# Optimization experiments

Hardware: AMD Instinct MI355X
Metric: run time of the kernel (lower is better)

## Reference

```python
import jax, jax.numpy as jnp
import numpy as np

D_INNER = 4096
DT_RANK = 128
D_STATE = 16
SEQ_LEN = 4096


def setup_inputs() -> dict:
    key = jax.random.key(0)
    kx, kin, kdel = jax.random.split(key, 3)
    x = jax.random.normal(kx, (SEQ_LEN, D_INNER), dtype=jnp.float32)
    # eqx.nn.Linear weights are [out_features, in_features]
    lim_in = 1.0 / np.sqrt(D_INNER)
    W_in = jax.random.uniform(kin, (DT_RANK + 2 * D_STATE, D_INNER),
                              minval=-lim_in, maxval=lim_in, dtype=jnp.float32)
    lim_d = 1.0 / np.sqrt(DT_RANK)
    W_delta = jax.random.uniform(kdel, (D_INNER, DT_RANK),
                                 minval=-lim_d, maxval=lim_d, dtype=jnp.float32)
    # A_log init exactly as in the module (deterministic)
    A = jnp.repeat(jnp.arange(1, D_STATE + 1), D_INNER).reshape(D_INNER, D_STATE)
    A_log = jnp.log(A.astype(jnp.float32))
    D = jnp.ones((D_INNER,), dtype=jnp.float32)
    return {"x": x, "W_in": W_in, "W_delta": W_delta, "A_log": A_log, "D": D}


def selective_scan(x, delta, A, B, C, D):
    # x, delta: [L, d_inner]; A: [d_inner, d_state]; B, C: [L, d_state]; D: [d_inner]
    d_inner, d_state = A.shape
    delta_A = jnp.exp(jnp.einsum('ld,dn->ldn', delta, A))          # [L, d_inner, d_state]
    delta_B_u = jnp.einsum('ld,ln,ld->ldn', delta, B, x)           # [L, d_inner, d_state]

    def step(h, inp):
        dA, dBu, c = inp
        h = dA * h + dBu                                           # [d_inner, d_state]
        y = jnp.einsum('dn,n->d', h, c)
        return h, y

    h0 = jnp.zeros((d_inner, d_state), dtype=x.dtype)
    _, ys = jax.lax.scan(step, h0, (delta_A, delta_B_u, C))
    return ys + x * D


def reference(x, W_in, W_delta, A_log, D):
    A = -jnp.exp(A_log)
    dbc = x @ W_in.T                                               # [L, dt_rank + 2*d_state]
    delta, B, C = jnp.split(dbc, [DT_RANK, DT_RANK + D_STATE], axis=-1)
    delta = jax.nn.softplus(delta @ W_delta.T)                     # [L, d_inner]
    return selective_scan(x, delta, A, B, C, D)
```

## Files before the change

### kernel.cpp

```cpp
#include <hip/hip_runtime.h>
#include <math.h>
#include <stdint.h>

#define L_SEQ   4096
#define DI      4096
#define RNK     128
#define NS      16
#define NCOL    160
#define KSPLIT  16

#define DBC_SLICE 655360
#define PART_OFF  655360
#define DSZ       524288
#define WSZ       655360
#define PART_STRIDE (32 * 4096)

typedef __attribute__((ext_vector_type(8))) short bf16x8;
typedef __attribute__((ext_vector_type(4))) float f32x4;

__device__ __forceinline__ float fast_exp2(float v) {
#if __has_builtin(__builtin_amdgcn_exp2f)
  return __builtin_amdgcn_exp2f(v);
#else
  return exp2f(v);
#endif
}

__device__ __forceinline__ unsigned short f2bf(float f) {
  uint32_t u = __float_as_uint(f);
  uint32_t r = (u + 0x7FFFu + ((u >> 16) & 1u)) >> 16;
  return (unsigned short)r;
}
__device__ __forceinline__ float bf2f(unsigned short b) {
  return __uint_as_float(((uint32_t)b) << 16);
}

__global__ __launch_bounds__(256) void split_pair_kernel(const float* __restrict__ src,
                                                         unsigned short* __restrict__ dh,
                                                         unsigned short* __restrict__ dl) {
  const int i = (blockIdx.x * 256 + threadIdx.x) * 4;
  float4 a = *(const float4*)&src[i];
  float v[4] = {a.x, a.y, a.z, a.w};
  ushort4 h, lo;
  unsigned short* hp = (unsigned short*)&h;
  unsigned short* lp = (unsigned short*)&lo;
#pragma unroll
  for (int q = 0; q < 4; ++q) {
    hp[q] = f2bf(v[q]);
    lp[q] = f2bf(v[q] - bf2f(hp[q]));
  }
  *(ushort4*)&dh[i] = h;
  *(ushort4*)&dl[i] = lo;
}

__global__ __launch_bounds__(256) void gemm1_kernel(const float* __restrict__ x,
                                                    const unsigned short* __restrict__ winh,
                                                    const unsigned short* __restrict__ winl,
                                                    float* __restrict__ parts) {
  const int t  = threadIdx.x;
  const int w  = t >> 6, l = t & 63;
  const int lr = l & 15;
  const int lk = l >> 4;
  const int mt = blockIdx.x >> 4;
  const int ks = blockIdx.x & 15;
  const int wr = w >> 1, wc = w & 1;
  const int row = mt * 32 + wr * 16 + lr;
  const int c0  = wc * 80;
  const int kb  = ks * 256;

  f32x4 acc[5];
#pragma unroll
  for (int j = 0; j < 5; ++j) acc[j] = (f32x4){0.f, 0.f, 0.f, 0.f};

#pragma unroll
  for (int kc = 0; kc < 8; ++kc) {
    const int k0 = kb + kc * 32 + lk * 8;
    float4 xa0 = *(const float4*)&x[row * 4096 + k0];
    float4 xa1 = *(const float4*)&x[row * 4096 + k0 + 4];
    float va[8] = {xa0.x, xa0.y, xa0.z, xa0.w, xa1.x, xa1.y, xa1.z, xa1.w};
    bf16x8 ah, al_;
#pragma unroll
    for (int q = 0; q < 8; ++q) {
      unsigned short hq = f2bf(va[q]);
      ah[q]  = (short)hq;
      al_[q] = (short)f2bf(va[q] - bf2f(hq));
    }
#pragma unroll
    for (int j = 0; j < 5; ++j) {
      const int col = c0 + j * 16 + lr;
      bf16x8 bh = *(const bf16x8*)&winh[col * 4096 + k0];
      bf16x8 bl = *(const bf16x8*)&winl[col * 4096 + k0];
      acc[j] = __builtin_amdgcn_mfma_f32_16x16x32_bf16(ah,  bh, acc[j], 0, 0, 0);
      acc[j] = __builtin_amdgcn_mfma_f32_16x16x32_bf16(ah,  bl, acc[j], 0, 0, 0);
      acc[j] = __builtin_amdgcn_mfma_f32_16x16x32_bf16(al_, bh, acc[j], 0, 0, 0);
    }
  }

  float* outp = parts + ks * DBC_SLICE;
  const int r0 = mt * 32 + wr * 16 + lk * 4;
#pragma unroll
  for (int j = 0; j < 5; ++j)
#pragma unroll
    for (int r = 0; r < 4; ++r)
      outp[(r0 + r) * NCOL + c0 + j * 16 + lr] = acc[j][r];
}

__global__ __launch_bounds__(256) void reduce_dbc_kernel(const float* __restrict__ parts,
                                                         float* __restrict__ dbc,
                                                         unsigned short* __restrict__ dbch,
                                                         unsigned short* __restrict__ dbcl) {
  const int i = (blockIdx.x * 256 + threadIdx.x) * 4;
  float4 a = *(const float4*)&parts[i];
#pragma unroll
  for (int s = 1; s < KSPLIT; ++s) {
    float4 b = *(const float4*)&parts[(size_t)s * DBC_SLICE + i];
    a.x += b.x; a.y += b.y; a.z += b.z; a.w += b.w;
  }
  const int row = i / NCOL;
  const int col = i - row * NCOL;
  if (col < RNK) {
    float v[4] = {a.x, a.y, a.z, a.w};
    ushort4 h, lo;
    unsigned short* hp = (unsigned short*)&h;
    unsigned short* lp = (unsigned short*)&lo;
#pragma unroll
    for (int q = 0; q < 4; ++q) {
      hp[q] = f2bf(v[q]);
      lp[q] = f2bf(v[q] - bf2f(hp[q]));
    }
    *(ushort4*)&dbch[row * RNK + col] = h;
    *(ushort4*)&dbcl[row * RNK + col] = lo;
  } else {
    *(float4*)&dbc[i] = a;
  }
}

__global__ __launch_bounds__(256) void gemm2_kernel(const unsigned short* __restrict__ dbch,
                                                    const unsigned short* __restrict__ dbcl,
                                                    const unsigned short* __restrict__ Wdh,
                                                    const unsigned short* __restrict__ Wdl,
                                                    float* __restrict__ delta_out) {
  const int t  = threadIdx.x;
  const int w  = t >> 6, l = t & 63;
  const int lr = l & 15;
  const int lk = l >> 4;
  const int mt = blockIdx.x & 63, nt = blockIdx.x >> 6;
  const int wr = w >> 1, wc = w & 1;
  const int m0 = mt * 64 + wr * 32;
  const int n0 = nt * 128 + wc * 64;

  f32x4 acc[2][4];
#pragma unroll
  for (int i = 0; i < 2; ++i)
#pragma unroll
    for (int j = 0; j < 4; ++j)
      acc[i][j] = (f32x4){0.f, 0.f, 0.f, 0.f};

#pragma unroll
  for (int ks = 0; ks < 4; ++ks) {
    const int k0 = ks * 32 + lk * 8;
    bf16x8 ah[2], al_[2], bh[4], bl[4];
#pragma unroll
    for (int i = 0; i < 2; ++i) {
      ah[i]  = *(const bf16x8*)&dbch[(m0 + i * 16 + lr) * RNK + k0];
      al_[i] = *(const bf16x8*)&dbcl[(m0 + i * 16 + lr) * RNK + k0];
    }
#pragma unroll
    for (int j = 0; j < 4; ++j) {
      bh[j] = *(const bf16x8*)&Wdh[(n0 + j * 16 + lr) * RNK + k0];
      bl[j] = *(const bf16x8*)&Wdl[(n0 + j * 16 + lr) * RNK + k0];
    }
#pragma unroll
    for (int i = 0; i < 2; ++i)
#pragma unroll
      for (int j = 0; j < 4; ++j) {
        acc[i][j] = __builtin_amdgcn_mfma_f32_16x16x32_bf16(ah[i],  bh[j], acc[i][j], 0, 0, 0);
        acc[i][j] = __builtin_amdgcn_mfma_f32_16x16x32_bf16(ah[i],  bl[j], acc[i][j], 0, 0, 0);
        acc[i][j] = __builtin_amdgcn_mfma_f32_16x16x32_bf16(al_[i], bh[j], acc[i][j], 0, 0, 0);
      }
  }

#pragma unroll
  for (int i = 0; i < 2; ++i)
#pragma unroll
    for (int j = 0; j < 4; ++j)
#pragma unroll
      for (int r = 0; r < 4; ++r) {
        const int row = m0 + i * 16 + lk * 4 + r;
        const int col = n0 + j * 16 + lr;
        float v = acc[i][j][r];
        float sp = (v > 20.f) ? v : log1pf(__expf(v));
        delta_out[row * 4096 + col] = sp;
      }
}

template <int CLEN_T>
__global__ __launch_bounds__(256) void scan1_kernel(const float* __restrict__ delta,
                                                    const float* __restrict__ x,
                                                    const float* __restrict__ A_log,
                                                    const float* __restrict__ dbc,
                                                    float* __restrict__ part) {
  __shared__ float Bs[CLEN_T][NS];
  const int t = threadIdx.x;
  const int d = blockIdx.x * 256 + t;
  const int g = blockIdx.y;
  const int l0 = g * CLEN_T;
#pragma unroll
  for (int i = 0; i < CLEN_T * NS / 256; ++i) {
    int f = t + i * 256;
    int l = f >> 4, n = f & 15;
    Bs[l][n] = dbc[(l0 + l) * NCOL + RNK + n];
  }
  __syncthreads();

  float al2[NS];
#pragma unroll
  for (int n = 0; n < NS; ++n) al2[n] = -expf(A_log[d * NS + n]) * 1.44269504f;
  bool uni = true;
#pragma unroll
  for (int n = 1; n < NS; ++n) uni = uni && (al2[n] == al2[0]);

  float h[NS], P[NS];
#pragma unroll
  for (int n = 0; n < NS; ++n) { h[n] = 0.f; P[n] = 1.f; }

  if (uni) {
    const float a0 = al2[0];
    float Ps = 1.f;
    for (int l = 0; l < CLEN_T; ++l) {
      float dv = delta[(l0 + l) * 4096 + d];
      float xv = x[(l0 + l) * 4096 + d];
      float dx = dv * xv;
      float dA = fast_exp2(dv * a0);
      Ps *= dA;
      const float4* br = (const float4*)Bs[l];
      float4 b0 = br[0], b1 = br[1], b2 = br[2], b3 = br[3];
      h[0]  = fmaf(dA, h[0],  dx * b0.x); h[1]  = fmaf(dA, h[1],  dx * b0.y);
      h[2]  = fmaf(dA, h[2],  dx * b0.z); h[3]  = fmaf(dA, h[3],  dx * b0.w);
      h[4]  = fmaf(dA, h[4],  dx * b1.x); h[5]  = fmaf(dA, h[5],  dx * b1.y);
      h[6]  = fmaf(dA, h[6],  dx * b1.z); h[7]  = fmaf(dA, h[7],  dx * b1.w);
      h[8]  = fmaf(dA, h[8],  dx * b2.x); h[9]  = fmaf(dA, h[9],  dx * b2.y);
      h[10] = fmaf(dA, h[10], dx * b2.z); h[11] = fmaf(dA, h[11], dx * b2.w);
      h[12] = fmaf(dA, h[12], dx * b3.x); h[13] = fmaf(dA, h[13], dx * b3.y);
      h[14] = fmaf(dA, h[14], dx * b3.z); h[15] = fmaf(dA, h[15], dx * b3.w);
    }
#pragma unroll
    for (int n = 0; n < NS; ++n) P[n] = Ps;
  } else {
    for (int l = 0; l < CLEN_T; ++l) {
      float dv = delta[(l0 + l) * 4096 + d];
      float xv = x[(l0 + l) * 4096 + d];
      float dx = dv * xv;
#pragma unroll
      for (int n = 0; n < NS; ++n) {
        float dA = fast_exp2(dv * al2[n]);
        h[n] = fmaf(dA, h[n], dx * Bs[l][n]);
        P[n] *= dA;
      }
    }
  }
  float* pg = part + (size_t)g * PART_STRIDE;
#pragma unroll
  for (int n = 0; n < NS; ++n) {
    pg[n * 4096 + d] = P[n];
    pg[(NS + n) * 4096 + d] = h[n];
  }
}

__global__ __launch_bounds__(256) void scan2_kernel(float* __restrict__ part, int gch) {
  const int idx = blockIdx.x * 256 + threadIdx.x;
  const int d = idx & 4095;
  const int n = idx >> 12;
  float h = 0.f;
  for (int g = 0; g < gch; ++g) {
    float* pg = part + (size_t)g * PART_STRIDE;
    float Pv = pg[n * 4096 + d];
    float Hv = pg[(NS + n) * 4096 + d];
    float nh = fmaf(Pv, h, Hv);
    pg[n * 4096 + d] = h;
    h = nh;
  }
}

template <int CLEN_T>
__global__ __launch_bounds__(256) void scan3_kernel(float* io,
                                                    const float* __restrict__ x,
                                                    const float* __restrict__ A_log,
                                                    const float* __restrict__ dbc,
                                                    const float* __restrict__ Dvec,
                                                    const float* __restrict__ part) {
  __shared__ float Bs[CLEN_T][NS];
  __shared__ float Cs[CLEN_T][NS];
  const int t = threadIdx.x;
  const int d = blockIdx.x * 256 + t;
  const int g = blockIdx.y;
  const int l0 = g * CLEN_T;
#pragma unroll
  for (int i = 0; i < CLEN_T * NS / 256; ++i) {
    int f = t + i * 256;
    int l = f >> 4, n = f & 15;
    Bs[l][n] = dbc[(l0 + l) * NCOL + RNK + n];
    Cs[l][n] = dbc[(l0 + l) * NCOL + RNK + NS + n];
  }
  __syncthreads();

  float al2[NS];
#pragma unroll
  for (int n = 0; n < NS; ++n) al2[n] = -expf(A_log[d * NS + n]) * 1.44269504f;
  bool uni = true;
#pragma unroll
  for (int n = 1; n < NS; ++n) uni = uni && (al2[n] == al2[0]);

  float h[NS];
  const float* pg = part + (size_t)g * PART_STRIDE;
#pragma unroll
  for (int n = 0; n < NS; ++n) h[n] = pg[n * 4096 + d];
  const float Dd = Dvec[d];

  if (uni) {
    const float a0 = al2[0];
    for (int l = 0; l < CLEN_T; ++l) {
      float dv = io[(size_t)(l0 + l) * 4096 + d];
      float xv = x[(l0 + l) * 4096 + d];
      float dx = dv * xv;
      float dA = fast_exp2(dv * a0);
      const float4* br = (const float4*)Bs[l];
      const float4* cr = (const float4*)Cs[l];
      float4 b0 = br[0], b1 = br[1], b2 = br[2], b3 = br[3];
      float4 c0 = cr[0], c1 = cr[1], c2 = cr[2], c3 = cr[3];
      float y = 0.f;
      h[0]  = fmaf(dA, h[0],  dx * b0.x); y = fmaf(h[0],  c0.x, y);
      h[1]  = fmaf(dA, h[1],  dx * b0.y); y = fmaf(h[1],  c0.y, y);
      h[2]  = fmaf(dA, h[2],  dx * b0.z); y = fmaf(h[2],  c0.z, y);
      h[3]  = fmaf(dA, h[3],  dx * b0.w); y = fmaf(h[3],  c0.w, y);
      h[4]  = fmaf(dA, h[4],  dx * b1.x); y = fmaf(h[4],  c1.x, y);
      h[5]  = fmaf(dA, h[5],  dx * b1.y); y = fmaf(h[5],  c1.y, y);
      h[6]  = fmaf(dA, h[6],  dx * b1.z); y = fmaf(h[6],  c1.z, y);
      h[7]  = fmaf(dA, h[7],  dx * b1.w); y = fmaf(h[7],  c1.w, y);
      h[8]  = fmaf(dA, h[8],  dx * b2.x); y = fmaf(h[8],  c2.x, y);
      h[9]  = fmaf(dA, h[9],  dx * b2.y); y = fmaf(h[9],  c2.y, y);
      h[10] = fmaf(dA, h[10], dx * b2.z); y = fmaf(h[10], c2.z, y);
      h[11] = fmaf(dA, h[11], dx * b2.w); y = fmaf(h[11], c2.w, y);
      h[12] = fmaf(dA, h[12], dx * b3.x); y = fmaf(h[12], c3.x, y);
      h[13] = fmaf(dA, h[13], dx * b3.y); y = fmaf(h[13], c3.y, y);
      h[14] = fmaf(dA, h[14], dx * b3.z); y = fmaf(h[14], c3.z, y);
      h[15] = fmaf(dA, h[15], dx * b3.w); y = fmaf(h[15], c3.w, y);
      io[(size_t)(l0 + l) * 4096 + d] = fmaf(xv, Dd, y);
    }
  } else {
    for (int l = 0; l < CLEN_T; ++l) {
      float dv = io[(size_t)(l0 + l) * 4096 + d];
      float xv = x[(l0 + l) * 4096 + d];
      float dx = dv * xv;
      float y = 0.f;
#pragma unroll
      for (int n = 0; n < NS; ++n) {
        float dA = fast_exp2(dv * al2[n]);
        h[n] = fmaf(dA, h[n], dx * Bs[l][n]);
        y = fmaf(h[n], Cs[l][n], y);
      }
      io[(size_t)(l0 + l) * 4096 + d] = fmaf(xv, Dd, y);
    }
  }
}

extern "C" void kernel_launch(void* const* d_in, const int* in_sizes, int n_in,
                              void* d_out, int out_size, void* d_ws, size_t ws_size,
                              hipStream_t stream) {
  const float* x    = (const float*)d_in[0];
  const float* Win  = (const float*)d_in[1];
  const float* Wd   = (const float*)d_in[2];
  const float* Alog = (const float*)d_in[3];
  const float* Dv   = (const float*)d_in[4];
  float* out = (float*)d_out;
  float* ws  = (float*)d_ws;
  float* dbc  = ws;
  float* part = ws + PART_OFF;
  unsigned short* dbch = (unsigned short*)(ws + PART_OFF);
  unsigned short* dbcl = dbch + DSZ;
  unsigned short* wdh  = dbcl + DSZ;
  unsigned short* wdl  = wdh + DSZ;
  unsigned short* winh = wdl + DSZ;
  unsigned short* winl = winh + WSZ;

  const bool big = ws_size >= (size_t)(PART_OFF + 64 * PART_STRIDE) * sizeof(float);

  split_pair_kernel<<<640, 256, 0, stream>>>(Win, winh, winl);
  split_pair_kernel<<<512, 256, 0, stream>>>(Wd, wdh, wdl);
  gemm1_kernel<<<2048, 256, 0, stream>>>(x, winh, winl, out);
  reduce_dbc_kernel<<<640, 256, 0, stream>>>(out, dbc, dbch, dbcl);
  gemm2_kernel<<<2048, 256, 0, stream>>>(dbch, dbcl, wdh, wdl, out);
  if (big) {
    scan1_kernel<64><<<dim3(16, 64), 256, 0, stream>>>(out, x, Alog, dbc, part);
    scan2_kernel<<<256, 256, 0, stream>>>(part, 64);
    scan3_kernel<64><<<dim3(16, 64), 256, 0, stream>>>(out, x, Alog, dbc, Dv, part);
  } else {
    scan1_kernel<128><<<dim3(16, 32), 256, 0, stream>>>(out, x, Alog, dbc, part);
    scan2_kernel<<<256, 256, 0, stream>>>(part, 32);
    scan3_kernel<128><<<dim3(16, 32), 256, 0, stream>>>(out, x, Alog, dbc, Dv, part);
  }
}
```

Measured before the change: 370.4 us.

## Stage x and W_in tiles in LDS for gemm1 with 64-row blocks

The first projection GEMM now stages the x tile (split into bf16 hi/lo once per block) and the W_in hi/lo tiles in shared memory, and each block computes 64 rows by all 160 columns. Before, each wave reloaded W_in from global memory and each thread re-split its own x elements. The grid is halved, each wave holds 10 accumulators, and two barriers per k-chunk are added. The intent is to cut redundant global W_in traffic and duplicated conversion work, at the cost of LDS use, synchronisation and possibly lower occupancy.

```diff
diff --git a/kernel.cpp b/kernel.cpp
--- a/kernel.cpp
+++ b/kernel.cpp
@@ -57,52 +57,72 @@
                                                     const unsigned short* __restrict__ winh,
                                                     const unsigned short* __restrict__ winl,
                                                     float* __restrict__ parts) {
+  __shared__ unsigned short xw[2][224][40];
   const int t  = threadIdx.x;
   const int w  = t >> 6, l = t & 63;
   const int lr = l & 15;
   const int lk = l >> 4;
   const int mt = blockIdx.x >> 4;
   const int ks = blockIdx.x & 15;
-  const int wr = w >> 1, wc = w & 1;
-  const int row = mt * 32 + wr * 16 + lr;
-  const int c0  = wc * 80;
-  const int kb  = ks * 256;
-
-  f32x4 acc[5];
-#pragma unroll
-  for (int j = 0; j < 5; ++j) acc[j] = (f32x4){0.f, 0.f, 0.f, 0.f};
-
-#pragma unroll
+  const int row0 = mt * 64;
+  const int kbase0 = ks * 256;
+
+  f32x4 acc[10];
+#pragma unroll
+  for (int j = 0; j < 10; ++j) acc[j] = (f32x4){0.f, 0.f, 0.f, 0.f};
+
   for (int kc = 0; kc < 8; ++kc) {
-    const int k0 = kb + kc * 32 + lk * 8;
-    float4 xa0 = *(const float4*)&x[row * 4096 + k0];
-    float4 xa1 = *(const float4*)&x[row * 4096 + k0 + 4];
-    float va[8] = {xa0.x, xa0.y, xa0.z, xa0.w, xa1.x, xa1.y, xa1.z, xa1.w};
-    bf16x8 ah, al_;
-#pragma unroll
-    for (int q = 0; q < 8; ++q) {
-      unsigned short hq = f2bf(va[q]);
-      ah[q]  = (short)hq;
-      al_[q] = (short)f2bf(va[q] - bf2f(hq));
-    }
-#pragma unroll
-    for (int j = 0; j < 5; ++j) {
-      const int col = c0 + j * 16 + lr;
-      bf16x8 bh = *(const bf16x8*)&winh[col * 4096 + k0];
-      bf16x8 bl = *(const bf16x8*)&winl[col * 4096 + k0];
+    const int kb = kbase0 + kc * 32;
+#pragma unroll
+    for (int i = 0; i < 2; ++i) {
+      const int f = t + i * 256;
+      const int row = f >> 3, q = f & 7;
+      float4 v = *(const float4*)&x[(row0 + row) * 4096 + kb + q * 4];
+      float va[4] = {v.x, v.y, v.z, v.w};
+      ushort4 h, lo;
+      unsigned short* hp = (unsigned short*)&h;
+      unsigned short* lp = (unsigned short*)&lo;
+#pragma unroll
+      for (int qq = 0; qq < 4; ++qq) {
+        hp[qq] = f2bf(va[qq]);
+        lp[qq] = f2bf(va[qq] - bf2f(hp[qq]));
+      }
+      *(ushort4*)&xw[0][row][q * 4] = h;
+      *(ushort4*)&xw[1][row][q * 4] = lo;
+    }
+#pragma unroll
+    for (int i = 0; i < 5; ++i) {
+      const int f = t + i * 256;
+      const int ar = (f >= 640);
+      const int g  = f - ar * 640;
+      const int col = g >> 2, q = g & 3;
+      const unsigned short* src = ar ? winl : winh;
+      uint4 v = *(const uint4*)&src[col * 4096 + kb + q * 8];
+      *(uint4*)&xw[ar][64 + col][q * 8] = v;
+    }
+    __syncthreads();
+    const int rl = w * 16 + lr;
+    bf16x8 ah  = *(const bf16x8*)&xw[0][rl][lk * 8];
+    bf16x8 al_ = *(const bf16x8*)&xw[1][rl][lk * 8];
+#pragma unroll
+    for (int j = 0; j < 10; ++j) {
+      const int cl = 64 + j * 16 + lr;
+      bf16x8 bh = *(const bf16x8*)&xw[0][cl][lk * 8];
+      bf16x8 bl = *(const bf16x8*)&xw[1][cl][lk * 8];
       acc[j] = __builtin_amdgcn_mfma_f32_16x16x32_bf16(ah,  bh, acc[j], 0, 0, 0);
       acc[j] = __builtin_amdgcn_mfma_f32_16x16x32_bf16(ah,  bl, acc[j], 0, 0, 0);
       acc[j] = __builtin_amdgcn_mfma_f32_16x16x32_bf16(al_, bh, acc[j], 0, 0, 0);
     }
+    __syncthreads();
   }
 
   float* outp = parts + ks * DBC_SLICE;
-  const int r0 = mt * 32 + wr * 16 + lk * 4;
-#pragma unroll
-  for (int j = 0; j < 5; ++j)
+  const int r0 = mt * 64 + w * 16 + lk * 4;
+#pragma unroll
+  for (int j = 0; j < 10; ++j)
 #pragma unroll
     for (int r = 0; r < 4; ++r)
-      outp[(r0 + r) * NCOL + c0 + j * 16 + lr] = acc[j][r];
+      outp[(r0 + r) * NCOL + j * 16 + lr] = acc[j][r];
 }
 
 __global__ __launch_bounds__(256) void reduce_dbc_kernel(const float* __restrict__ parts,
@@ -387,7 +407,7 @@
 
   split_pair_kernel<<<640, 256, 0, stream>>>(Win, winh, winl);
   split_pair_kernel<<<512, 256, 0, stream>>>(Wd, wdh, wdl);
-  gemm1_kernel<<<2048, 256, 0, stream>>>(x, winh, winl, out);
+  gemm1_kernel<<<1024, 256, 0, stream>>>(x, winh, winl, out);
   reduce_dbc_kernel<<<640, 256, 0, stream>>>(out, dbc, dbch, dbcl);
   gemm2_kernel<<<2048, 256, 0, stream>>>(dbch, dbcl, wdh, wdl, out);
   if (big) {
```

Result: faster. 303.3 us (-18.1%).
